# Performance work log

Measured on AMD Instinct MI355X. Metric: run time of the kernel, lower is better.

Reference implementation:

```python
import jax, jax.numpy as jnp
import numpy as np

B, T, DIM = 8, 1024, 2048
H, NKV, HD = 16, 4, 128
G = H // NKV          # query heads per kv head
BASE = 10000.0
EPS = 1e-6
SCALE = HD ** -0.5


def _rope_tables(seqlen):
    inv = 1.0 / (BASE ** (np.arange(0, HD, 2, dtype=np.float32) / HD))  # [HD/2]
    t = np.arange(seqlen, dtype=np.float32)
    f = np.outer(t, inv)  # [T, HD/2]
    return jnp.asarray(np.cos(f)), jnp.asarray(np.sin(f))


def _rms_norm(x):
    return x * jax.lax.rsqrt(jnp.mean(x * x, axis=-1, keepdims=True) + EPS)


def _rope(x, cos, sin):
    # x: [B, heads, T, HD]; cos/sin broadcast over batch and heads
    x1, x2 = x[..., : HD // 2], x[..., HD // 2 :]
    return jnp.concatenate([x1 * cos - x2 * sin, x2 * cos + x1 * sin], axis=-1)


def setup_inputs() -> dict:
    key = jax.random.key(0)
    ks = jax.random.split(key, 6)
    s = 1.0 / np.sqrt(DIM)
    return {
        "x": jax.random.normal(ks[0], (B, T, DIM), dtype=jnp.float32),
        "Wq": jax.random.normal(ks[1], (DIM, DIM), dtype=jnp.float32) * s,
        "Wk": jax.random.normal(ks[2], (NKV * HD, DIM), dtype=jnp.float32) * s,
        "Wv": jax.random.normal(ks[3], (NKV * HD, DIM), dtype=jnp.float32) * s,
        "Wproj": jax.random.normal(ks[4], (DIM, DIM), dtype=jnp.float32) * s,
        "q_gain": jnp.ones((H,), dtype=jnp.float32),
    }


def reference(x, Wq, Wk, Wv, Wproj, q_gain):
    bsz, seqlen, dim = x.shape
    # projections -> [B, heads, T, HD]
    q = (x @ Wq.T).reshape(bsz, seqlen, H, HD).transpose(0, 2, 1, 3)
    k = (x @ Wk.T).reshape(bsz, seqlen, NKV, HD).transpose(0, 2, 1, 3)
    v = (x @ Wv.T).reshape(bsz, seqlen, NKV, HD).transpose(0, 2, 1, 3)

    cos, sin = _rope_tables(seqlen)
    cos, sin = cos[None, None], sin[None, None]
    q = _rope(_rms_norm(q), cos, sin) * q_gain[None, :, None, None]
    k = _rope(_rms_norm(k), cos, sin)

    # GQA: group query heads instead of materializing repeated k/v
    qg = q.reshape(bsz, NKV, G, seqlen, HD)
    scores = jnp.einsum("bngtd,bnsd->bngts", qg, k) * SCALE  # [B,NKV,G,T,T]
    causal = jnp.tril(jnp.ones((seqlen, seqlen), dtype=bool))
    scores = jnp.where(causal, scores, jnp.finfo(scores.dtype).min)
    p = jax.nn.softmax(scores, axis=-1)
    y = jnp.einsum("bngts,bnsd->bngtd", p, v)  # [B,NKV,G,T,HD]
    y = y.transpose(0, 3, 1, 2, 4).reshape(bsz, seqlen, dim)

    # XSA: subtract self-value projection per kv head
    y_g = y.reshape(bsz, seqlen, NKV, G, HD)
    v_t = v.transpose(0, 2, 1, 3)  # [B,T,NKV,HD]
    vn = v_t / (jnp.linalg.norm(v_t, axis=-1, keepdims=True) + 1e-8)
    vn = vn[:, :, :, None, :]  # broadcast over group dim
    proj_comp = jnp.sum(y_g * vn, axis=-1, keepdims=True) * vn
    y = (y_g - proj_comp).reshape(bsz, seqlen, dim)

    return y @ Wproj.T
```

## Files before the change

### kernel.cpp

```cpp
#include <hip/hip_runtime.h>
#include <stdint.h>

#define T_SEQ 1024

typedef _Float16 f16x8 __attribute__((ext_vector_type(8)));
typedef float f32x4 __attribute__((ext_vector_type(4)));

typedef __attribute__((address_space(1))) const uint8_t* gptr_t;
typedef __attribute__((address_space(3))) uint8_t* lptr_t;

__device__ __forceinline__ void gload16(const _Float16* g, _Float16* l) {
  __builtin_amdgcn_global_load_lds((gptr_t)g, (lptr_t)l, 16, 0, 0);
}

__global__ __launch_bounds__(256) void convert_all(
    const float* __restrict__ x, const float* __restrict__ Wq,
    const float* __restrict__ Wk, const float* __restrict__ Wv,
    const float* __restrict__ Wp, _Float16* __restrict__ xh,
    _Float16* __restrict__ wqh, _Float16* __restrict__ wkh,
    _Float16* __restrict__ wvh, _Float16* __restrict__ wph) {
  int i = blockIdx.x * 256 + threadIdx.x;
  const float* in;
  _Float16* out;
  int base;
  if (i < 2097152)      { in = x;  out = xh;  base = 0; }
  else if (i < 2621440) { in = Wq; out = wqh; base = 2097152; }
  else if (i < 2752512) { in = Wk; out = wkh; base = 2621440; }
  else if (i < 2883584) { in = Wv; out = wvh; base = 2752512; }
  else                  { in = Wp; out = wph; base = 2883584; }
  int j = i - base;
  const float4* p = (const float4*)in + (size_t)j * 2;
  float4 a = p[0], b = p[1];
  f16x8 o;
  o[0] = (_Float16)a.x; o[1] = (_Float16)a.y; o[2] = (_Float16)a.z; o[3] = (_Float16)a.w;
  o[4] = (_Float16)b.x; o[5] = (_Float16)b.y; o[6] = (_Float16)b.z; o[7] = (_Float16)b.w;
  ((f16x8*)out)[j] = o;
}

template <typename OutT>
__global__ __launch_bounds__(512, 2) void gemm256(
    const _Float16* __restrict__ A, const _Float16* __restrict__ B,
    OutT* __restrict__ C0, int ldc0, int nb0,
    OutT* __restrict__ C1, int ldc1, int nbn) {
  __shared__ _Float16 As[2][256][64];
  __shared__ _Float16 Bs[2][256][64];
  const int tid = threadIdx.x;
  const int wave = tid >> 6, lane = tid & 63;
  const int lm = lane & 15, lq = lane >> 4;
  const int wm = wave >> 2, wn = wave & 3;

  const int qx = (int)gridDim.x >> 3;
  const int swz = ((int)blockIdx.x & 7) * qx + ((int)blockIdx.x >> 3);
  const int bm = swz / nbn, bn = swz % nbn;

  const int r8 = lane >> 3;
  const int csw = ((lane & 7) ^ r8) * 8;
  const _Float16* Asrc = A + (size_t)(bm * 256 + wave * 16 + r8) * 2048 + csw;
  const _Float16* Bsrc = B + (size_t)(bn * 256 + wave * 16 + r8) * 2048 + csw;

  f32x4 acc[8][4];
#pragma unroll
  for (int m = 0; m < 8; m++)
#pragma unroll
    for (int n = 0; n < 4; n++) acc[m][n] = (f32x4){0.f, 0.f, 0.f, 0.f};

  f16x8 af[4][2], bf[4][2];

  auto stageA = [&](int t, int h) {
    const _Float16* s = Asrc + (size_t)h * 128 * 2048 + t * 64;
    _Float16* d = &As[t & 1][h * 128 + wave * 16][0];
    gload16(s, d);
    gload16(s + (size_t)8 * 2048, d + 8 * 64);
  };
  auto stageB = [&](int t, int h) {
    const _Float16* s = Bsrc + (size_t)h * 128 * 2048 + t * 64;
    _Float16* d = &Bs[t & 1][h * 128 + wave * 16][0];
    gload16(s, d);
    gload16(s + (size_t)8 * 2048, d + 8 * 64);
  };
  auto lda = [&](int b, int mh) {
#pragma unroll
    for (int m = 0; m < 4; m++)
#pragma unroll
      for (int ks = 0; ks < 2; ks++)
        af[m][ks] = *(const f16x8*)&As[b][wm * 128 + mh * 64 + m * 16 + lm]
                                      [(((ks * 4 + lq)) ^ (lm & 7)) * 8];
  };
  auto ldb = [&](int b, int nh) {
#pragma unroll
    for (int n = 0; n < 2; n++)
#pragma unroll
      for (int ks = 0; ks < 2; ks++)
        bf[nh * 2 + n][ks] = *(const f16x8*)&Bs[b][wn * 64 + nh * 32 + n * 16 + lm]
                                               [(((ks * 4 + lq)) ^ (lm & 7)) * 8];
  };
  auto mfmaQ = [&](int mh, int nh) {
    __builtin_amdgcn_s_setprio(1);
#pragma unroll
    for (int m = 0; m < 4; m++)
#pragma unroll
      for (int n = 0; n < 2; n++)
#pragma unroll
        for (int ks = 0; ks < 2; ks++)
          acc[mh * 4 + m][nh * 2 + n] = __builtin_amdgcn_mfma_f32_16x16x32_f16(
              af[m][ks], bf[nh * 2 + n][ks], acc[mh * 4 + m][nh * 2 + n], 0, 0, 0);
    __builtin_amdgcn_s_setprio(0);
  };

#define BAR() __builtin_amdgcn_s_barrier()
#define LGKM0() asm volatile("s_waitcnt lgkmcnt(0)" ::: "memory")

  stageA(0, 0); stageA(0, 1);
  stageB(0, 0); stageB(0, 1);
  stageB(1, 0); stageB(1, 1);
  asm volatile("s_waitcnt vmcnt(4)" ::: "memory");
  BAR();

  const int NT = 32;
  for (int j = 0; j < NT / 2; ++j) {
    const int t1 = 2 * j + 1, t2 = 2 * j + 2, t3 = 2 * j + 3;
    const bool s2 = t2 < NT, s3 = t3 < NT;
    lda(0, 0); ldb(0, 0); stageA(t1, 0);
    BAR(); LGKM0(); mfmaQ(0, 0); BAR();
    ldb(0, 1); stageA(t1, 1);
    BAR(); LGKM0(); mfmaQ(0, 1); BAR();
    lda(0, 1); if (s2) stageB(t2, 0);
    BAR(); LGKM0(); mfmaQ(1, 0); BAR();
    if (s2) stageB(t2, 1);
    BAR(); mfmaQ(1, 1);
    if (s2) { asm volatile("s_waitcnt vmcnt(4)" ::: "memory"); }
    else    { asm volatile("s_waitcnt vmcnt(0)" ::: "memory"); }
    BAR();
    lda(1, 0); ldb(1, 0); if (s2) stageA(t2, 0);
    BAR(); LGKM0(); mfmaQ(0, 0); BAR();
    ldb(1, 1); if (s2) stageA(t2, 1);
    BAR(); LGKM0(); mfmaQ(0, 1); BAR();
    lda(1, 1); if (s3) stageB(t3, 0);
    BAR(); LGKM0(); mfmaQ(1, 0); BAR();
    if (s3) stageB(t3, 1);
    BAR(); mfmaQ(1, 1);
    asm volatile("s_waitcnt vmcnt(4)" ::: "memory");
    BAR();
  }
#undef BAR
#undef LGKM0

  OutT* C;
  int ldc, cb;
  if (bn < nb0) { C = C0; ldc = ldc0; cb = bn * 256; }
  else          { C = C1; ldc = ldc1; cb = (bn - nb0) * 256; }
#pragma unroll
  for (int m = 0; m < 8; m++) {
    size_t gr = (size_t)(bm * 256 + wm * 128 + m * 16 + lq * 4);
#pragma unroll
    for (int n = 0; n < 4; n++) {
      int gc = cb + wn * 64 + n * 16 + lm;
#pragma unroll
      for (int r = 0; r < 4; r++)
        C[(gr + r) * ldc + gc] = (OutT)acc[m][n][r];
    }
  }
}

__global__ __launch_bounds__(256) void transpose16(const _Float16* __restrict__ in,
                                                   _Float16* __restrict__ out) {
  __shared__ _Float16 Ts[64][72];
  int tr = blockIdx.x * 64, tc = blockIdx.y * 64;
  int r0 = threadIdx.x >> 3, c8 = (threadIdx.x & 7) * 8;
#pragma unroll
  for (int i = 0; i < 2; i++) {
    int r = r0 + i * 32;
    *(f16x8*)&Ts[r][c8] = *(const f16x8*)&in[(size_t)(tr + r) * 1024 + tc + c8];
  }
  __syncthreads();
#pragma unroll
  for (int i = 0; i < 2; i++) {
    int oc = r0 + i * 32;
    f16x8 o;
#pragma unroll
    for (int j = 0; j < 8; j++) o[j] = Ts[c8 + j][oc];
    *(f16x8*)&out[(size_t)(tc + oc) * 8192 + tr + c8] = o;
  }
}

__global__ __launch_bounds__(256) void rmsrope_all(_Float16* __restrict__ qh,
                                                   _Float16* __restrict__ kvb,
                                                   const float* __restrict__ gain) {
  int gw = blockIdx.x * 4 + (threadIdx.x >> 6);
  int lane = threadIdx.x & 63;
  _Float16* row;
  int t;
  float g = 1.0f;
  if (gw < 131072) {
    int h = gw & 15;
    t = (gw >> 4) & 1023;
    row = qh + (size_t)gw * 128;
    g = gain[h] * 0.08838834764831845f * 1.4426950408889634f;
  } else {
    int gk = gw - 131072;
    t = (gk >> 2) & 1023;
    row = kvb + (size_t)(gk >> 2) * 1024 + (gk & 3) * 128;
  }
  float x1 = (float)row[lane], x2 = (float)row[lane + 64];
  float ss = x1 * x1 + x2 * x2;
#pragma unroll
  for (int m = 1; m < 64; m <<= 1) ss += __shfl_xor(ss, m);
  float scale = rsqrtf(ss * (1.0f / 128.0f) + 1e-6f) * g;
  float inv = exp2f((float)lane * -0.2076205059304601f);
  float ang = (float)t * inv;
  float c = cosf(ang), s = sinf(ang);
  row[lane]      = (_Float16)((x1 * c - x2 * s) * scale);
  row[lane + 64] = (_Float16)((x2 * c + x1 * s) * scale);
}

__global__ __launch_bounds__(256, 2) void attn_mfma(const _Float16* __restrict__ q,
                                                    const _Float16* __restrict__ k,
                                                    const _Float16* __restrict__ vT,
                                                    _Float16* __restrict__ y) {
  __shared__ _Float16 Ks[4][64][32];
  __shared__ _Float16 VTs[2][128][32];
  __shared__ _Float16 Ps[4][32][64];
  int h = blockIdx.y, b = blockIdx.z;
  int kvh = h >> 2;
  int tid = threadIdx.x, wave = tid >> 6, lane = tid & 63;
  int lm = lane & 15, lq = lane >> 4;
  int srow = lane >> 2, scol = (lane & 3) * 8;

  for (int pass = 0; pass < 2; ++pass) {
    int qt = pass ? (int)blockIdx.x : 7 - (int)blockIdx.x;

    f16x8 qf[2][4];
#pragma unroll
    for (int mt = 0; mt < 2; mt++) {
      const _Float16* qp =
          q + ((size_t)((b * T_SEQ + qt * 128 + wave * 32 + mt * 16 + lm) * 16 + h)) * 128 +
          lq * 8;
#pragma unroll
      for (int ks = 0; ks < 4; ks++) qf[mt][ks] = *(const f16x8*)(qp + ks * 32);
    }

    f32x4 O[2][8];
#pragma unroll
    for (int mt = 0; mt < 2; mt++)
#pragma unroll
      for (int i = 0; i < 8; i++) O[mt][i] = (f32x4){0.f, 0.f, 0.f, 0.f};
    float mrow[2][4], lrow[2][4];
#pragma unroll
    for (int mt = 0; mt < 2; mt++)
#pragma unroll
      for (int r = 0; r < 4; r++) { mrow[mt][r] = -1e30f; lrow[mt][r] = 0.f; }

    const _Float16* kg =
        k + (size_t)(b * T_SEQ + srow) * 1024 + kvh * 128 + wave * 32 + scol;
    const _Float16* vg =
        vT + (size_t)(kvh * 128 + (wave >> 1) * 64 + srow) * 8192 + b * T_SEQ +
        (wave & 1) * 32 + scol;

    int wrow = qt * 128 + wave * 32;
    int smax = qt * 128 + 128;
    for (int s0 = 0; s0 < smax; s0 += 64) {
#pragma unroll
      for (int i = 0; i < 4; i++) {
        gload16(kg + (size_t)i * 16 * 1024, &Ks[wave][i * 16][0]);
        gload16(vg + (size_t)i * 16 * 8192, &VTs[wave & 1][(wave >> 1) * 64 + i * 16][0]);
      }
      kg += (size_t)64 * 1024;
      vg += 64;
      __syncthreads();

      f32x4 S[2][4];
#pragma unroll
      for (int mt = 0; mt < 2; mt++)
#pragma unroll
        for (int ct = 0; ct < 4; ct++) S[mt][ct] = (f32x4){0.f, 0.f, 0.f, 0.f};
#pragma unroll
      for (int ct = 0; ct < 4; ct++)
#pragma unroll
        for (int ks = 0; ks < 4; ks++) {
          f16x8 bfr = *(const f16x8*)&Ks[ks][ct * 16 + lm][lq * 8];
          S[0][ct] = __builtin_amdgcn_mfma_f32_16x16x32_f16(qf[0][ks], bfr, S[0][ct], 0, 0, 0);
          S[1][ct] = __builtin_amdgcn_mfma_f32_16x16x32_f16(qf[1][ks], bfr, S[1][ct], 0, 0, 0);
        }

      float p[2][4][4], al[2][4];
#pragma unroll
      for (int mt = 0; mt < 2; mt++) {
        bool need_mask = (s0 + 63 > wrow + mt * 16);
#pragma unroll
        for (int r = 0; r < 4; r++) {
          int grow = wrow + mt * 16 + lq * 4 + r;
          float mx = -1e30f;
#pragma unroll
          for (int ct = 0; ct < 4; ct++) {
            float sv = S[mt][ct][r];
            if (need_mask && (s0 + ct * 16 + lm > grow)) sv = -1e30f;
            p[mt][r][ct] = sv;
            mx = fmaxf(mx, sv);
          }
#pragma unroll
          for (int m = 1; m < 16; m <<= 1) mx = fmaxf(mx, __shfl_xor(mx, m));
          float mn = fmaxf(mrow[mt][r], mx);
          float a = exp2f(mrow[mt][r] - mn);
          mrow[mt][r] = mn;
          float rs = 0.f;
#pragma unroll
          for (int ct = 0; ct < 4; ct++) {
            float pv = exp2f(p[mt][r][ct] - mn);
            p[mt][r][ct] = pv;
            rs += pv;
          }
#pragma unroll
          for (int m = 1; m < 16; m <<= 1) rs += __shfl_xor(rs, m);
          lrow[mt][r] = lrow[mt][r] * a + rs;
          al[mt][r] = a;
        }
      }

#pragma unroll
      for (int mt = 0; mt < 2; mt++)
#pragma unroll
        for (int r = 0; r < 4; r++) {
          int prow = mt * 16 + lq * 4 + r;
#pragma unroll
          for (int ct = 0; ct < 4; ct++) {
            int cg = (ct * 2 + (lm >> 3)) ^ (prow & 7);
            Ps[wave][prow][cg * 8 + (lm & 7)] = (_Float16)p[mt][r][ct];
          }
        }
#pragma unroll
      for (int mt = 0; mt < 2; mt++)
#pragma unroll
        for (int ct = 0; ct < 8; ct++)
#pragma unroll
          for (int r = 0; r < 4; r++) O[mt][ct][r] *= al[mt][r];

#pragma unroll
      for (int ks2 = 0; ks2 < 2; ks2++) {
        f16x8 afr[2];
#pragma unroll
        for (int mt = 0; mt < 2; mt++) {
          int prow = mt * 16 + lm;
          int cg = (ks2 * 4 + lq) ^ (prow & 7);
          afr[mt] = *(const f16x8*)&Ps[wave][prow][cg * 8];
        }
#pragma unroll
        for (int ct = 0; ct < 8; ct++) {
          f16x8 bfr = *(const f16x8*)&VTs[ks2][ct * 16 + lm][lq * 8];
          O[0][ct] = __builtin_amdgcn_mfma_f32_16x16x32_f16(afr[0], bfr, O[0][ct], 0, 0, 0);
          O[1][ct] = __builtin_amdgcn_mfma_f32_16x16x32_f16(afr[1], bfr, O[1][ct], 0, 0, 0);
        }
      }
      __syncthreads();
    }

#pragma unroll
    for (int mt = 0; mt < 2; mt++) {
      float linv[4];
#pragma unroll
      for (int r = 0; r < 4; r++) linv[r] = 1.0f / lrow[mt][r];
      int qrow_base = wrow + mt * 16 + lq * 4;
#pragma unroll
      for (int ct = 0; ct < 8; ct++)
#pragma unroll
        for (int r = 0; r < 4; r++)
          y[((size_t)(b * T_SEQ + qrow_base + r) * 16 + h) * 128 + ct * 16 + lm] =
              (_Float16)(O[mt][ct][r] * linv[r]);
    }
  }
}

__global__ __launch_bounds__(256) void vreject(const _Float16* __restrict__ y,
                                               const _Float16* __restrict__ kvb,
                                               _Float16* __restrict__ yh) {
  int gw = blockIdx.x * 4 + (threadIdx.x >> 6);
  int lane = threadIdx.x & 63;
  int bt = gw >> 2, n = gw & 3;
  const _Float16* vrow = kvb + (size_t)bt * 1024 + 512 + n * 128;
  float v1 = (float)vrow[lane], v2 = (float)vrow[lane + 64];
  float ss = v1 * v1 + v2 * v2;
#pragma unroll
  for (int m = 1; m < 64; m <<= 1) ss += __shfl_xor(ss, m);
  float invn = 1.0f / (sqrtf(ss) + 1e-8f);
  float n1 = v1 * invn, n2 = v2 * invn;
  const _Float16* ybase = y + (size_t)bt * 2048 + n * 512;
  _Float16* obase = yh + (size_t)bt * 2048 + n * 512;
#pragma unroll
  for (int g = 0; g < 4; g++) {
    float y1 = (float)ybase[g * 128 + lane], y2 = (float)ybase[g * 128 + lane + 64];
    float d = y1 * n1 + y2 * n2;
#pragma unroll
    for (int m = 1; m < 64; m <<= 1) d += __shfl_xor(d, m);
    obase[g * 128 + lane]      = (_Float16)(y1 - d * n1);
    obase[g * 128 + lane + 64] = (_Float16)(y2 - d * n2);
  }
}

extern "C" void kernel_launch(void* const* d_in, const int* in_sizes, int n_in,
                              void* d_out, int out_size, void* d_ws, size_t ws_size,
                              hipStream_t stream) {
  const float* x    = (const float*)d_in[0];
  const float* Wq   = (const float*)d_in[1];
  const float* Wk   = (const float*)d_in[2];
  const float* Wv   = (const float*)d_in[3];
  const float* Wp   = (const float*)d_in[4];
  const float* gain = (const float*)d_in[5];
  float* out = (float*)d_out;

  char* w = (char*)d_ws;
  _Float16* xh   = (_Float16*)(w + 0);
  _Float16* wqh  = (_Float16*)(w + 32u * 1048576);
  _Float16* wkvh = (_Float16*)(w + 40u * 1048576);
  _Float16* wph  = (_Float16*)(w + 44u * 1048576);
  _Float16* qh   = (_Float16*)(w + 52u * 1048576);
  _Float16* kvb  = (_Float16*)(w + 84u * 1048576);
  _Float16* vTg  = (_Float16*)(w + 100u * 1048576);
  _Float16* ya   = (_Float16*)(w + 108u * 1048576);
  _Float16* yh2  = xh;

  convert_all<<<13312, 256, 0, stream>>>(x, Wq, Wk, Wv, Wp, xh, wqh,
                                         wkvh, wkvh + (size_t)512 * 2048, wph);

  gemm256<_Float16><<<384, 512, 0, stream>>>(xh, wqh, qh, 2048, 8, kvb, 1024, 12);

  transpose16<<<dim3(128, 8), 256, 0, stream>>>(kvb + 512, vTg);
  rmsrope_all<<<40960, 256, 0, stream>>>(qh, kvb, gain);

  attn_mfma<<<dim3(4, 16, 8), 256, 0, stream>>>(qh, kvb, vTg, ya);

  vreject<<<8192, 256, 0, stream>>>(ya, kvb, yh2);

  gemm256<float><<<256, 512, 0, stream>>>(yh2, wph, out, 2048, 8,
                                          (float*)nullptr, 2048, 8);
}
```

Before: 484.1 us.

## Double-buffer K/V tiles in attention kernel to overlap loads with MFMA

Adds a second LDS buffer for the K and V^T tiles and prefetches the next 64-key tile with global_load_lds while the current tile is processed, so there is one barrier per iteration. This is meant to hide global-memory latency behind the QK and PV MFMA work. LDS use rises from about 40KB to 64KB per block, which may limit how many blocks fit per CU under launch_bounds(256,2). The explicit vmcnt(0) wait plus s_barrier replaces __syncthreads.

Result: no change. 485.1 us (+0.2%).

```diff
diff --git a/kernel.cpp b/kernel.cpp
--- a/kernel.cpp
+++ b/kernel.cpp
@@ -217,8 +217,8 @@
                                                     const _Float16* __restrict__ k,
                                                     const _Float16* __restrict__ vT,
                                                     _Float16* __restrict__ y) {
-  __shared__ _Float16 Ks[4][64][32];
-  __shared__ _Float16 VTs[2][128][32];
+  __shared__ _Float16 Ks[2][4][64][32];
+  __shared__ _Float16 VTs[2][2][128][32];
   __shared__ _Float16 Ps[4][32][64];
   int h = blockIdx.y, b = blockIdx.z;
   int kvh = h >> 2;
@@ -257,16 +257,31 @@
         (wave & 1) * 32 + scol;
 
     int wrow = qt * 128 + wave * 32;
-    int smax = qt * 128 + 128;
-    for (int s0 = 0; s0 < smax; s0 += 64) {
-#pragma unroll
-      for (int i = 0; i < 4; i++) {
-        gload16(kg + (size_t)i * 16 * 1024, &Ks[wave][i * 16][0]);
-        gload16(vg + (size_t)i * 16 * 8192, &VTs[wave & 1][(wave >> 1) * 64 + i * 16][0]);
+    int nit = (qt + 1) * 2;
+
+#pragma unroll
+    for (int i = 0; i < 4; i++) {
+      gload16(kg + (size_t)i * 16 * 1024, &Ks[0][wave][i * 16][0]);
+      gload16(vg + (size_t)i * 16 * 8192, &VTs[0][wave & 1][(wave >> 1) * 64 + i * 16][0]);
+    }
+    kg += (size_t)64 * 1024;
+    vg += 64;
+    asm volatile("s_waitcnt vmcnt(0)" ::: "memory");
+    __builtin_amdgcn_s_barrier();
+
+    for (int it = 0; it < nit; ++it) {
+      int cur = it & 1;
+      int s0 = it * 64;
+      if (it + 1 < nit) {
+#pragma unroll
+        for (int i = 0; i < 4; i++) {
+          gload16(kg + (size_t)i * 16 * 1024, &Ks[cur ^ 1][wave][i * 16][0]);
+          gload16(vg + (size_t)i * 16 * 8192,
+                  &VTs[cur ^ 1][wave & 1][(wave >> 1) * 64 + i * 16][0]);
+        }
+        kg += (size_t)64 * 1024;
+        vg += 64;
       }
-      kg += (size_t)64 * 1024;
-      vg += 64;
-      __syncthreads();
 
       f32x4 S[2][4];
 #pragma unroll
@@ -277,7 +292,7 @@
       for (int ct = 0; ct < 4; ct++)
 #pragma unroll
         for (int ks = 0; ks < 4; ks++) {
-          f16x8 bfr = *(const f16x8*)&Ks[ks][ct * 16 + lm][lq * 8];
+          f16x8 bfr = *(const f16x8*)&Ks[cur][ks][ct * 16 + lm][lq * 8];
           S[0][ct] = __builtin_amdgcn_mfma_f32_16x16x32_f16(qf[0][ks], bfr, S[0][ct], 0, 0, 0);
           S[1][ct] = __builtin_amdgcn_mfma_f32_16x16x32_f16(qf[1][ks], bfr, S[1][ct], 0, 0, 0);
         }
@@ -345,12 +360,13 @@
         }
 #pragma unroll
         for (int ct = 0; ct < 8; ct++) {
-          f16x8 bfr = *(const f16x8*)&VTs[ks2][ct * 16 + lm][lq * 8];
+          f16x8 bfr = *(const f16x8*)&VTs[cur][ks2][ct * 16 + lm][lq * 8];
           O[0][ct] = __builtin_amdgcn_mfma_f32_16x16x32_f16(afr[0], bfr, O[0][ct], 0, 0, 0);
           O[1][ct] = __builtin_amdgcn_mfma_f32_16x16x32_f16(afr[1], bfr, O[1][ct], 0, 0, 0);
         }
       }
-      __syncthreads();
+      asm volatile("s_waitcnt vmcnt(0)" ::: "memory");
+      __builtin_amdgcn_s_barrier();
     }
 
 #pragma unroll
```
